# Optimization experiments

Hardware: AMD Instinct MI355X
Metric: run time of the kernel (lower is better)

## Reference

```python
import jax, jax.numpy as jnp
import numpy as np

EPS = 1e-12  # torch F.normalize eps


def setup_inputs() -> dict:
    key = jax.random.key(0)
    k1, k2, k3 = jax.random.split(key, 3)
    N, C, H, W = 64, 512, 30, 30
    K = 64
    x = jax.random.normal(k1, (N, C, H, W), dtype=jnp.float32)
    conv_w = jax.random.normal(k2, (K, C), dtype=jnp.float32) * 0.02
    centroids = jax.random.uniform(k3, (K, C), dtype=jnp.float32)
    return {"x": x, "conv_w": conv_w, "centroids": centroids}


def reference(x, conv_w, centroids):
    N, C, H, W = x.shape
    K = conv_w.shape[0]
    # descriptor-wise L2 normalization over channel dim (torch F.normalize, p=2, dim=1)
    norm = jnp.sqrt(jnp.sum(x * x, axis=1, keepdims=True))
    x = x / jnp.maximum(norm, EPS)
    xf = x.reshape(N, C, H * W)  # [N, C, P]
    # 1x1 conv (no bias) -> logits [N, K, P]; softmax over clusters K
    logits = jnp.einsum("ncp,kc->nkp", xf, conv_w)
    a = jax.nn.softmax(logits, axis=1)  # [N, K, P]
    # vlad[n,k,c] = sum_p a[n,k,p] * (x[n,c,p] - centroids[k,c])
    #            = (a @ x^T)[n,k,c] - centroids[k,c] * sum_p a[n,k,p]
    vlad = jnp.einsum("nkp,ncp->nkc", a, xf) - a.sum(axis=-1)[:, :, None] * centroids[None]
    return vlad
```

## Files before the change

kernel.cpp:

```cpp
#include <hip/hip_runtime.h>

typedef __attribute__((ext_vector_type(8))) __bf16 bf16x8;
typedef __attribute__((ext_vector_type(4))) float f32x4;

namespace {
constexpr int N_ = 64, C_ = 512, P_ = 900, K_ = 64;
constexpr int PP = 960;
constexpr size_t TOT_X = (size_t)N_ * C_ * P_;
constexpr size_t AT_BYTES  = (size_t)N_ * K_ * PP * 2;
constexpr size_t ASUM_OFF  = AT_BYTES;
constexpr size_t WB_OFF    = ASUM_OFF + (size_t)N_ * K_ * 4;
}

__global__ __launch_bounds__(256) void k_prep_w(const float* __restrict__ w,
                                                __bf16* __restrict__ wb) {
  int i = (blockIdx.x * 256 + threadIdx.x) * 4;
  if (i < K_ * C_) {
    float4 v = *reinterpret_cast<const float4*>(w + i);
    wb[i]   = (__bf16)v.x; wb[i+1] = (__bf16)v.y;
    wb[i+2] = (__bf16)v.z; wb[i+3] = (__bf16)v.w;
  }
}

__global__ __launch_bounds__(256) void k_phase1(const float* __restrict__ x,
                                                const __bf16* __restrict__ wb,
                                                __bf16* __restrict__ at,
                                                float* __restrict__ asum) {
  __shared__ __bf16 Xb[4][64][8];
  __shared__ float ssq_l[64];
  __shared__ float Sw[64][5];
  const int n   = blockIdx.y;
  const int p0  = blockIdx.x * 64;
  const int tid = threadIdx.x;
  const int w   = tid >> 6, l = tid & 63;
  const int l15 = l & 15,  lh = l >> 4;

  bf16x8 afr[16];
  #pragma unroll
  for (int s = 0; s < 16; ++s)
    afr[s] = *reinterpret_cast<const bf16x8*>(
        wb + (size_t)(16 * w + l15) * C_ + s * 32 + lh * 8);

  f32x4 acc[4] = {};
  float sq[4] = {0.f, 0.f, 0.f, 0.f};
  if (tid < 64) ssq_l[tid] = 0.f;

  const int pq = (tid & 15) * 4;
  #pragma unroll
  for (int s = 0; s < 16; ++s) {
    __syncthreads();
    #pragma unroll
    for (int it = 0; it < 2; ++it) {
      const int idx = tid + it * 256;
      const int c = idx >> 4;
      size_t off = ((size_t)n * C_ + s * 32 + c) * P_ + p0 + pq;
      if (off > TOT_X - 4) off = TOT_X - 4;
      const float4 v = *reinterpret_cast<const float4*>(x + off);
      sq[0] = fmaf(v.x, v.x, sq[0]); sq[1] = fmaf(v.y, v.y, sq[1]);
      sq[2] = fmaf(v.z, v.z, sq[2]); sq[3] = fmaf(v.w, v.w, sq[3]);
      __bf16* dst = &Xb[c >> 3][pq][c & 7];
      dst[0]  = (__bf16)v.x; dst[8]  = (__bf16)v.y;
      dst[16] = (__bf16)v.z; dst[24] = (__bf16)v.w;
    }
    __syncthreads();
    #pragma unroll
    for (int t = 0; t < 4; ++t) {
      bf16x8 b = *reinterpret_cast<const bf16x8*>(&Xb[lh][16 * t + l15][0]);
      acc[t] = __builtin_amdgcn_mfma_f32_16x16x32_bf16(afr[s], b, acc[t], 0, 0, 0);
    }
  }

  #pragma unroll
  for (int q = 0; q < 4; ++q) atomicAdd(&ssq_l[pq + q], sq[q]);
  __syncthreads();

  float invn[4], invs_[4];
  bool valid[4];
  #pragma unroll
  for (int t = 0; t < 4; ++t) {
    invn[t] = 1.f / fmaxf(sqrtf(ssq_l[16 * t + l15]), 1e-12f);
    valid[t] = (p0 + 16 * t + l15) < P_;
    float ps = 0.f;
    #pragma unroll
    for (int r = 0; r < 4; ++r) {
      acc[t][r] = __expf(acc[t][r] * invn[t]);
      ps += acc[t][r];
    }
    ps += __shfl_xor(ps, 16, 64);
    ps += __shfl_xor(ps, 32, 64);
    if (l < 16) Sw[16 * t + l][w] = ps;
  }
  __syncthreads();
  #pragma unroll
  for (int t = 0; t < 4; ++t) {
    float S = Sw[16 * t + l15][0] + Sw[16 * t + l15][1] +
              Sw[16 * t + l15][2] + Sw[16 * t + l15][3];
    invs_[t] = 1.f / S;
  }

  #pragma unroll
  for (int t = 0; t < 4; ++t) {
    const int p = p0 + 16 * t + l15;
    #pragma unroll
    for (int r = 0; r < 4; ++r) {
      const int k = 16 * w + lh * 4 + r;
      const float ar = acc[t][r] * invs_[t];
      at[((size_t)n * K_ + k) * PP + p] = valid[t] ? (__bf16)(ar * invn[t]) : (__bf16)0.f;
    }
  }
  #pragma unroll
  for (int r = 0; r < 4; ++r) {
    float v = 0.f;
    #pragma unroll
    for (int t = 0; t < 4; ++t)
      v += valid[t] ? acc[t][r] * invs_[t] : 0.f;
    v += __shfl_xor(v, 1, 64); v += __shfl_xor(v, 2, 64);
    v += __shfl_xor(v, 4, 64); v += __shfl_xor(v, 8, 64);
    if (l15 == 0)
      unsafeAtomicAdd(asum + n * K_ + 16 * w + lh * 4 + r, v);
  }
}

__global__ __launch_bounds__(256) void k_phase2(const float* __restrict__ x,
                                                const __bf16* __restrict__ at,
                                                const float* __restrict__ asum,
                                                const float* __restrict__ cent,
                                                float* __restrict__ out) {
  __shared__ __bf16 Al[64][40];
  __shared__ __bf16 Xl[64][40];
  const int n   = blockIdx.y;
  const int c0  = blockIdx.x * 64;
  const int tid = threadIdx.x;
  const int w   = tid >> 6, l = tid & 63;
  const int l15 = l & 15,  lh = l >> 4;

  f32x4 acc[4] = {};

  for (int s = 0; s < 29; ++s) {
    const int pb = s * 32;
    __syncthreads();
    {
      const int k = tid >> 2, ch = tid & 3;
      bf16x8 v = *reinterpret_cast<const bf16x8*>(
          at + ((size_t)n * K_ + k) * PP + pb + ch * 8);
      *reinterpret_cast<bf16x8*>(&Al[k][ch * 8]) = v;
    }
    #pragma unroll
    for (int it = 0; it < 2; ++it) {
      const int idx = tid + it * 256;
      const int c = idx >> 3, ch = idx & 7;
      size_t off = ((size_t)n * C_ + c0 + c) * P_ + pb + ch * 4;
      if (off > TOT_X - 4) off = TOT_X - 4;
      const float4 v = *reinterpret_cast<const float4*>(x + off);
      __bf16* d = &Xl[c][ch * 4];
      d[0] = (__bf16)v.x; d[1] = (__bf16)v.y;
      d[2] = (__bf16)v.z; d[3] = (__bf16)v.w;
    }
    __syncthreads();
    bf16x8 b = *reinterpret_cast<const bf16x8*>(&Xl[16 * w + l15][lh * 8]);
    #pragma unroll
    for (int m = 0; m < 4; ++m) {
      bf16x8 a = *reinterpret_cast<const bf16x8*>(&Al[16 * m + l15][lh * 8]);
      acc[m] = __builtin_amdgcn_mfma_f32_16x16x32_bf16(a, b, acc[m], 0, 0, 0);
    }
  }

  const int c = c0 + 16 * w + l15;
  #pragma unroll
  for (int m = 0; m < 4; ++m) {
    #pragma unroll
    for (int r = 0; r < 4; ++r) {
      const int k = 16 * m + lh * 4 + r;
      out[((size_t)n * K_ + k) * C_ + c] =
          acc[m][r] - asum[n * K_ + k] * cent[(size_t)k * C_ + c];
    }
  }
}

extern "C" void kernel_launch(void* const* d_in, const int* in_sizes, int n_in,
                              void* d_out, int out_size, void* d_ws, size_t ws_size,
                              hipStream_t stream) {
  const float* x    = (const float*)d_in[0];
  const float* w    = (const float*)d_in[1];
  const float* cent = (const float*)d_in[2];
  float* out = (float*)d_out;
  char* wsb  = (char*)d_ws;
  __bf16* at   = (__bf16*)wsb;
  float*  asum = (float*)(wsb + ASUM_OFF);
  __bf16* wb   = (__bf16*)(wsb + WB_OFF);

  hipMemsetAsync(asum, 0, (size_t)N_ * K_ * sizeof(float), stream);
  k_prep_w<<<dim3(32), dim3(256), 0, stream>>>(w, wb);
  k_phase1<<<dim3(15, 64), dim3(256), 0, stream>>>(x, wb, at, asum);
  k_phase2<<<dim3(8, 64), dim3(256), 0, stream>>>(x, at, asum, cent, out);
}
```

Baseline: 83.37 us.

## Double-buffer LDS tiles with register prefetch in both phases, fold memset into prep

```diff
diff --git a/kernel.cpp b/kernel.cpp
--- a/kernel.cpp
+++ b/kernel.cpp
@@ -1,6 +1,7 @@
 #include <hip/hip_runtime.h>
 
 typedef __attribute__((ext_vector_type(8))) __bf16 bf16x8;
+typedef __attribute__((ext_vector_type(4))) __bf16 bf16x4;
 typedef __attribute__((ext_vector_type(4))) float f32x4;
 
 namespace {
@@ -13,21 +14,24 @@
 }
 
 __global__ __launch_bounds__(256) void k_prep_w(const float* __restrict__ w,
-                                                __bf16* __restrict__ wb) {
-  int i = (blockIdx.x * 256 + threadIdx.x) * 4;
+                                                __bf16* __restrict__ wb,
+                                                float* __restrict__ asum) {
+  const int t = blockIdx.x * 256 + threadIdx.x;
+  const int i = t * 4;
   if (i < K_ * C_) {
     float4 v = *reinterpret_cast<const float4*>(w + i);
     wb[i]   = (__bf16)v.x; wb[i+1] = (__bf16)v.y;
     wb[i+2] = (__bf16)v.z; wb[i+3] = (__bf16)v.w;
   }
+  if (t < N_ * K_) asum[t] = 0.f;
 }
 
 __global__ __launch_bounds__(256) void k_phase1(const float* __restrict__ x,
                                                 const __bf16* __restrict__ wb,
                                                 __bf16* __restrict__ at,
                                                 float* __restrict__ asum) {
-  __shared__ __bf16 Xb[4][64][8];
-  __shared__ float ssq_l[64];
+  __shared__ __bf16 Xl[2][64][40];
+  __shared__ float SsqP[64][5];
   __shared__ float Sw[64][5];
   const int n   = blockIdx.y;
   const int p0  = blockIdx.x * 64;
@@ -41,45 +45,61 @@
     afr[s] = *reinterpret_cast<const bf16x8*>(
         wb + (size_t)(16 * w + l15) * C_ + s * 32 + lh * 8);
 
+  float nx[8];
+  float sq = 0.f;
+  const size_t xbase = (size_t)n * C_ * P_ + p0 + l;
+
   f32x4 acc[4] = {};
-  float sq[4] = {0.f, 0.f, 0.f, 0.f};
-  if (tid < 64) ssq_l[tid] = 0.f;
-
-  const int pq = (tid & 15) * 4;
+
+  #pragma unroll
+  for (int j = 0; j < 8; ++j) {
+    size_t off = xbase + (size_t)(w * 8 + j) * P_;
+    if (off > TOT_X - 1) off = TOT_X - 1;
+    nx[j] = x[off];
+  }
+  {
+    bf16x8 pk;
+    #pragma unroll
+    for (int j = 0; j < 8; ++j) { sq = fmaf(nx[j], nx[j], sq); pk[j] = (__bf16)nx[j]; }
+    *reinterpret_cast<bf16x8*>(&Xl[0][l][w * 8]) = pk;
+  }
+  __syncthreads();
+
   #pragma unroll
   for (int s = 0; s < 16; ++s) {
+    if (s < 15) {
+      #pragma unroll
+      for (int j = 0; j < 8; ++j) {
+        size_t off = xbase + (size_t)((s + 1) * 32 + w * 8 + j) * P_;
+        if (off > TOT_X - 1) off = TOT_X - 1;
+        nx[j] = x[off];
+      }
+    }
+    #pragma unroll
+    for (int t = 0; t < 4; ++t) {
+      bf16x8 b = *reinterpret_cast<const bf16x8*>(&Xl[s & 1][16 * t + l15][lh * 8]);
+      acc[t] = __builtin_amdgcn_mfma_f32_16x16x32_bf16(afr[s], b, acc[t], 0, 0, 0);
+    }
+    if (s < 15) {
+      bf16x8 pk;
+      #pragma unroll
+      for (int j = 0; j < 8; ++j) { sq = fmaf(nx[j], nx[j], sq); pk[j] = (__bf16)nx[j]; }
+      *reinterpret_cast<bf16x8*>(&Xl[(s + 1) & 1][l][w * 8]) = pk;
+    }
     __syncthreads();
-    #pragma unroll
-    for (int it = 0; it < 2; ++it) {
-      const int idx = tid + it * 256;
-      const int c = idx >> 4;
-      size_t off = ((size_t)n * C_ + s * 32 + c) * P_ + p0 + pq;
-      if (off > TOT_X - 4) off = TOT_X - 4;
-      const float4 v = *reinterpret_cast<const float4*>(x + off);
-      sq[0] = fmaf(v.x, v.x, sq[0]); sq[1] = fmaf(v.y, v.y, sq[1]);
-      sq[2] = fmaf(v.z, v.z, sq[2]); sq[3] = fmaf(v.w, v.w, sq[3]);
-      __bf16* dst = &Xb[c >> 3][pq][c & 7];
-      dst[0]  = (__bf16)v.x; dst[8]  = (__bf16)v.y;
-      dst[16] = (__bf16)v.z; dst[24] = (__bf16)v.w;
-    }
-    __syncthreads();
-    #pragma unroll
-    for (int t = 0; t < 4; ++t) {
-      bf16x8 b = *reinterpret_cast<const bf16x8*>(&Xb[lh][16 * t + l15][0]);
-      acc[t] = __builtin_amdgcn_mfma_f32_16x16x32_bf16(afr[s], b, acc[t], 0, 0, 0);
-    }
-  }
-
-  #pragma unroll
-  for (int q = 0; q < 4; ++q) atomicAdd(&ssq_l[pq + q], sq[q]);
+  }
+
+  SsqP[l][w] = sq;
   __syncthreads();
 
   float invn[4], invs_[4];
   bool valid[4];
   #pragma unroll
   for (int t = 0; t < 4; ++t) {
-    invn[t] = 1.f / fmaxf(sqrtf(ssq_l[16 * t + l15]), 1e-12f);
-    valid[t] = (p0 + 16 * t + l15) < P_;
+    const int pl = 16 * t + l15;
+    const float ss = SsqP[pl][0] + SsqP[pl][1] + SsqP[pl][2] + SsqP[pl][3];
+    invn[t] = 1.f / fmaxf(sqrtf(ss), 1e-12f);
+    valid[t] = (p0 + pl) < P_;
     float ps = 0.f;
     #pragma unroll
     for (int r = 0; r < 4; ++r) {
@@ -88,14 +108,13 @@
     }
     ps += __shfl_xor(ps, 16, 64);
     ps += __shfl_xor(ps, 32, 64);
-    if (l < 16) Sw[16 * t + l][w] = ps;
+    if (lh == 0) Sw[pl][w] = ps;
   }
   __syncthreads();
   #pragma unroll
   for (int t = 0; t < 4; ++t) {
-    float S = Sw[16 * t + l15][0] + Sw[16 * t + l15][1] +
-              Sw[16 * t + l15][2] + Sw[16 * t + l15][3];
-    invs_[t] = 1.f / S;
+    const int pl = 16 * t + l15;
+    invs_[t] = 1.f / (Sw[pl][0] + Sw[pl][1] + Sw[pl][2] + Sw[pl][3]);
   }
 
   #pragma unroll
@@ -126,43 +145,52 @@
                                                 const float* __restrict__ asum,
                                                 const float* __restrict__ cent,
                                                 float* __restrict__ out) {
-  __shared__ __bf16 Al[64][40];
-  __shared__ __bf16 Xl[64][40];
+  __shared__ __bf16 Al[2][64][40];
+  __shared__ __bf16 Xl[2][64][40];
   const int n   = blockIdx.y;
   const int c0  = blockIdx.x * 64;
   const int tid = threadIdx.x;
   const int w   = tid >> 6, l = tid & 63;
   const int l15 = l & 15,  lh = l >> 4;
 
+  const int ak  = tid >> 2, ach = tid & 3;
+  const int xc  = tid >> 3, xch = tid & 7;
+  const size_t abase = ((size_t)n * K_ + ak) * PP + ach * 8;
+  const size_t xbase0 = ((size_t)n * C_ + c0 + xc) * P_ + xch * 4;
+  const size_t xbase1 = ((size_t)n * C_ + c0 + xc + 32) * P_ + xch * 4;
+
   f32x4 acc[4] = {};
-
+  bf16x8 na; float4 v0, v1;
+
+  auto LOAD = [&](int s) {
+    na = *reinterpret_cast<const bf16x8*>(at + abase + s * 32);
+    size_t o0 = xbase0 + s * 32; if (o0 > TOT_X - 4) o0 = TOT_X - 4;
+    size_t o1 = xbase1 + s * 32; if (o1 > TOT_X - 4) o1 = TOT_X - 4;
+    v0 = *reinterpret_cast<const float4*>(x + o0);
+    v1 = *reinterpret_cast<const float4*>(x + o1);
+  };
+  auto STORE = [&](int b) {
+    *reinterpret_cast<bf16x8*>(&Al[b][ak][ach * 8]) = na;
+    bf16x4 p0 = { (__bf16)v0.x, (__bf16)v0.y, (__bf16)v0.z, (__bf16)v0.w };
+    bf16x4 p1 = { (__bf16)v1.x, (__bf16)v1.y, (__bf16)v1.z, (__bf16)v1.w };
+    *reinterpret_cast<bf16x4*>(&Xl[b][xc][xch * 4])      = p0;
+    *reinterpret_cast<bf16x4*>(&Xl[b][xc + 32][xch * 4]) = p1;
+  };
+
+  LOAD(0); STORE(0);
+  __syncthreads();
+
+  #pragma unroll 2
   for (int s = 0; s < 29; ++s) {
-    const int pb = s * 32;
+    if (s < 28) LOAD(s + 1);
+    bf16x8 b = *reinterpret_cast<const bf16x8*>(&Xl[s & 1][16 * w + l15][lh * 8]);
+    #pragma unroll
+    for (int m = 0; m < 4; ++m) {
+      bf16x8 a = *reinterpret_cast<const bf16x8*>(&Al[s & 1][16 * m + l15][lh * 8]);
+      acc[m] = __builtin_amdgcn_mfma_f32_16x16x32_bf16(a, b, acc[m], 0, 0, 0);
+    }
+    if (s < 28) STORE((s + 1) & 1);
     __syncthreads();
-    {
-      const int k = tid >> 2, ch = tid & 3;
-      bf16x8 v = *reinterpret_cast<const bf16x8*>(
-          at + ((size_t)n * K_ + k) * PP + pb + ch * 8);
-      *reinterpret_cast<bf16x8*>(&Al[k][ch * 8]) = v;
-    }
-    #pragma unroll
-    for (int it = 0; it < 2; ++it) {
-      const int idx = tid + it * 256;
-      const int c = idx >> 3, ch = idx & 7;
-      size_t off = ((size_t)n * C_ + c0 + c) * P_ + pb + ch * 4;
-      if (off > TOT_X - 4) off = TOT_X - 4;
-      const float4 v = *reinterpret_cast<const float4*>(x + off);
-      __bf16* d = &Xl[c][ch * 4];
-      d[0] = (__bf16)v.x; d[1] = (__bf16)v.y;
-      d[2] = (__bf16)v.z; d[3] = (__bf16)v.w;
-    }
-    __syncthreads();
-    bf16x8 b = *reinterpret_cast<const bf16x8*>(&Xl[16 * w + l15][lh * 8]);
-    #pragma unroll
-    for (int m = 0; m < 4; ++m) {
-      bf16x8 a = *reinterpret_cast<const bf16x8*>(&Al[16 * m + l15][lh * 8]);
-      acc[m] = __builtin_amdgcn_mfma_f32_16x16x32_bf16(a, b, acc[m], 0, 0, 0);
-    }
   }
 
   const int c = c0 + 16 * w + l15;
@@ -189,8 +217,7 @@
   float*  asum = (float*)(wsb + ASUM_OFF);
   __bf16* wb   = (__bf16*)(wsb + WB_OFF);
 
-  hipMemsetAsync(asum, 0, (size_t)N_ * K_ * sizeof(float), stream);
-  k_prep_w<<<dim3(32), dim3(256), 0, stream>>>(w, wb);
+  k_prep_w<<<dim3(32), dim3(256), 0, stream>>>(w, wb, asum);
   k_phase1<<<dim3(15, 64), dim3(256), 0, stream>>>(x, wb, at, asum);
   k_phase2<<<dim3(8, 64), dim3(256), 0, stream>>>(x, at, asum, cent, out);
 }
```

Measured after the change: 90.69 us. 8.8% more time.
